# Optimization experiments

Measured on AMD Instinct MI355X. Metric: run time of the kernel, lower is better.

The kernel has to match this reference:

```python
import jax, jax.numpy as jnp
import numpy as np

NEG_INF = -1e30


def setup_inputs() -> dict:
    key = jax.random.key(0)
    ks = jax.random.split(key, 5)
    B, S, D, H = 2, 2048, 1024, 16
    sc = 0.02  # weight init scale
    return {
        "x": jax.random.normal(ks[0], (B, S, D), dtype=jnp.float32),
        "Wq": jax.random.normal(ks[1], (D, D), dtype=jnp.float32) * sc,
        "bq": jnp.zeros((D,), dtype=jnp.float32),
        "Wk": jax.random.normal(ks[2], (D, D), dtype=jnp.float32) * sc,
        "bk": jnp.zeros((D,), dtype=jnp.float32),
        "Wv": jax.random.normal(ks[3], (D, D), dtype=jnp.float32) * sc,
        "bv": jnp.zeros((D,), dtype=jnp.float32),
        "Wo": jax.random.normal(ks[4], (D, D), dtype=jnp.float32) * sc,
        "bo": jnp.zeros((D,), dtype=jnp.float32),
        "temperature": jnp.ones((H,), dtype=jnp.float32),
    }


def reference(x, Wq, bq, Wk, bk, Wv, bv, Wo, bo, temperature):
    B, S, D = x.shape
    H = temperature.shape[0]
    hd = D // H
    sparsity = 0.8
    k = max(1, int(S * (1.0 - sparsity)))
    scale = hd ** (-0.5)

    # torch Linear: y = x @ W^T + b ; reshape to [B, S, H, hd] -> [B, H, S, hd]
    def proj(W, b):
        return (x @ W.T + b).reshape(B, S, H, hd).transpose(0, 2, 1, 3)

    q, kk, v = proj(Wq, bq), proj(Wk, bk), proj(Wv, bv)

    temp = jnp.clip(temperature, 0.1, None)[None, :, None, None]  # [1,H,1,1]
    scores = jnp.einsum("bhqd,bhkd->bhqk", q, kk) * scale / temp  # [B,H,S,S]

    # top-k sparsity: keep the k largest scores per row, -inf elsewhere.
    # Equivalent to torch's topk+scatter for distinct values: threshold at
    # the k-th largest value per row.
    topk_vals = jax.lax.top_k(scores, k)[0]           # [B,H,S,k]
    kth = topk_vals[..., -1:]                          # [B,H,S,1]
    sparse_scores = jnp.where(scores >= kth, scores, NEG_INF)

    attn = jax.nn.softmax(sparse_scores, axis=-1)      # [B,H,S,S]
    head_out = jnp.einsum("bhqk,bhkd->bhqd", attn, v)  # [B,H,S,hd]

    # stack heads back: [B,S,H,hd] -> [B,S,D], then out projection
    out = head_out.transpose(0, 2, 1, 3).reshape(B, S, D)
    out = out @ Wo.T + bo

    avg_attention = attn.mean(axis=1)                  # [B,S,S]
    return out, avg_attention
```

## Files before the change

kernel.cpp:

```cpp
#include <hip/hip_runtime.h>
#include <stdint.h>

#define S_LEN 2048
#define D_DIM 1024
#define NHEAD 16
#define HD    64
#define TOPK  409

typedef unsigned short u16;
typedef __attribute__((ext_vector_type(8))) short bf16x8;
typedef __attribute__((ext_vector_type(4))) float f32x4;
#define MFMA __builtin_amdgcn_mfma_f32_16x16x32_bf16

__device__ __forceinline__ u16 f2b(float f) {
    unsigned u = __float_as_uint(f);
    return (u16)((u + 0x7fffu + ((u >> 16) & 1u)) >> 16);
}
__device__ __forceinline__ float b2f(u16 h) {
    return __uint_as_float(((unsigned)h) << 16);
}

__global__ __launch_bounds__(256, 4)
void split_f32(const float* __restrict__ src, u16* __restrict__ hi,
               u16* __restrict__ lo, int n4)
{
    const int i = blockIdx.x * 256 + threadIdx.x;
    if (i >= n4) return;
    const float4 v = ((const float4*)src)[i];
    const float vv[4] = {v.x, v.y, v.z, v.w};
    u16 h4[4], l4[4];
#pragma unroll
    for (int c = 0; c < 4; ++c) {
        h4[c] = f2b(vv[c]);
        l4[c] = f2b(vv[c] - b2f(h4[c]));
    }
    ((ushort4*)hi)[i] = make_ushort4(h4[0], h4[1], h4[2], h4[3]);
    ((ushort4*)lo)[i] = make_ushort4(l4[0], l4[1], l4[2], l4[3]);
}

__global__ __launch_bounds__(256, 4)
void split4_f32(const float* __restrict__ s0, const float* __restrict__ s1,
                const float* __restrict__ s2, const float* __restrict__ s3,
                u16* __restrict__ h0, u16* __restrict__ l0,
                u16* __restrict__ h1, u16* __restrict__ l1,
                u16* __restrict__ h2, u16* __restrict__ l2,
                u16* __restrict__ h3, u16* __restrict__ l3, int n4)
{
    const int i = blockIdx.x * 256 + threadIdx.x;
    if (i >= n4) return;
    const int y = blockIdx.y;
    const float* src = (y == 0) ? s0 : (y == 1) ? s1 : (y == 2) ? s2 : s3;
    u16* hi = (y == 0) ? h0 : (y == 1) ? h1 : (y == 2) ? h2 : h3;
    u16* lo = (y == 0) ? l0 : (y == 1) ? l1 : (y == 2) ? l2 : l3;
    const float4 v = ((const float4*)src)[i];
    const float vv[4] = {v.x, v.y, v.z, v.w};
    u16 h4[4], l4[4];
#pragma unroll
    for (int c = 0; c < 4; ++c) {
        h4[c] = f2b(vv[c]);
        l4[c] = f2b(vv[c] - b2f(h4[c]));
    }
    ((ushort4*)hi)[i] = make_ushort4(h4[0], h4[1], h4[2], h4[3]);
    ((ushort4*)lo)[i] = make_ushort4(l4[0], l4[1], l4[2], l4[3]);
}

template<int MODE>
__global__ __launch_bounds__(512, 2)
void proj_mfma(const u16* __restrict__ Ahi, const u16* __restrict__ Alo,
               const u16* __restrict__ Whi, const u16* __restrict__ Wlo,
               const float* __restrict__ bias, float* __restrict__ outf,
               u16* __restrict__ o1, u16* __restrict__ o2)
{
    const int t = threadIdx.x, w = t >> 6, l = t & 63;
    const int lq = l & 15, quad = l >> 4;
    const int m0 = blockIdx.y * 128 + (w >> 2) * 64;
    const int n0 = blockIdx.x * 128 + (w & 3) * 32;

    f32x4 acc[4][2];
#pragma unroll
    for (int i = 0; i < 4; ++i)
#pragma unroll
        for (int j = 0; j < 2; ++j) acc[i][j] = (f32x4){0.f, 0.f, 0.f, 0.f};

    const size_t abase = (size_t)(m0 + lq) * D_DIM + quad * 8;
    const size_t bbase = (size_t)(n0 + lq) * D_DIM + quad * 8;

#pragma unroll 2
    for (int k0 = 0; k0 < D_DIM; k0 += 32) {
        bf16x8 ah[4], al[4], bh[2], bl[2];
#pragma unroll
        for (int i = 0; i < 4; ++i) {
            ah[i] = *(const bf16x8*)(Ahi + abase + (size_t)i * 16 * D_DIM + k0);
            al[i] = *(const bf16x8*)(Alo + abase + (size_t)i * 16 * D_DIM + k0);
        }
#pragma unroll
        for (int j = 0; j < 2; ++j) {
            bh[j] = *(const bf16x8*)(Whi + bbase + (size_t)j * 16 * D_DIM + k0);
            bl[j] = *(const bf16x8*)(Wlo + bbase + (size_t)j * 16 * D_DIM + k0);
        }
#pragma unroll
        for (int i = 0; i < 4; ++i)
#pragma unroll
            for (int j = 0; j < 2; ++j) {
                acc[i][j] = MFMA(ah[i], bh[j], acc[i][j], 0, 0, 0);
                acc[i][j] = MFMA(ah[i], bl[j], acc[i][j], 0, 0, 0);
                acc[i][j] = MFMA(al[i], bh[j], acc[i][j], 0, 0, 0);
            }
    }

#pragma unroll
    for (int j = 0; j < 2; ++j) {
        const int n = n0 + j * 16 + lq;
        const float bb = bias[n];
        const int hh = n >> 6, ee = n & 63;
#pragma unroll
        for (int i = 0; i < 4; ++i) {
            const int mb = m0 + i * 16 + quad * 4;
            const int bbm = mb >> 11, ss = mb & 2047;
            if (MODE == 2) {
#pragma unroll
                for (int r = 0; r < 4; ++r)
                    outf[(size_t)(mb + r) * D_DIM + n] = acc[i][j][r] + bb;
            } else if (MODE == 1) {
                ushort4 pk;
                pk.x = f2b(acc[i][j][0] + bb);
                pk.y = f2b(acc[i][j][1] + bb);
                pk.z = f2b(acc[i][j][2] + bb);
                pk.w = f2b(acc[i][j][3] + bb);
                *(ushort4*)(o1 + ((size_t)((bbm * NHEAD + hh) * HD + ee)) * S_LEN + ss) = pk;
            } else {
#pragma unroll
                for (int r = 0; r < 4; ++r) {
                    const float v = acc[i][j][r] + bb;
                    const size_t idx = ((size_t)(bbm * NHEAD + hh) * S_LEN + ss + r) * HD + ee;
                    const u16 h = f2b(v);
                    o1[idx] = h;
                    o2[idx] = f2b(v - b2f(h));
                }
            }
        }
    }
}

__global__ __launch_bounds__(512, 4)
void attn_mfma(const u16* __restrict__ Qhi, const u16* __restrict__ Qlo,
               const u16* __restrict__ Khi, const u16* __restrict__ Klo,
               const u16* __restrict__ Vt,  const float* __restrict__ temp,
               u16* __restrict__ HOhi, u16* __restrict__ HOlo,
               float* __restrict__ avg)
{
    __shared__ __align__(16) float sLds[8 * 2060];
    __shared__ float pvpart[4 * 16 * 16];

    const int t = threadIdx.x, w = t >> 6, l = t & 63;
    const int lq = l & 15, quad = l >> 4;
    const int b  = blockIdx.x >> 8;
    const int q0 = (blockIdx.x & 255) << 3;

    float avgreg[32];
#pragma unroll
    for (int i = 0; i < 32; ++i) avgreg[i] = 0.f;

#pragma unroll 1
    for (int h = 0; h < NHEAD; ++h) {
        const size_t bh = (size_t)(b * NHEAD + h) * S_LEN;
        const float tscale = 0.125f / fmaxf(temp[h], 0.1f);

        const u16* qph = Qhi + (bh + q0 + (lq & 7)) * HD + quad * 8;
        const u16* qpl = Qlo + (bh + q0 + (lq & 7)) * HD + quad * 8;
        const bf16x8 qh0 = *(const bf16x8*)qph;
        const bf16x8 qh1 = *(const bf16x8*)(qph + 32);
        const bf16x8 ql0 = *(const bf16x8*)qpl;
        const bf16x8 ql1 = *(const bf16x8*)(qpl + 32);

#pragma unroll 1
        for (int p = 0; p < 2; ++p) {
            f32x4 acc[8];
            const u16* kph = Khi + (bh + p * 1024 + w * 128 + lq) * HD + quad * 8;
            const u16* kpl = Klo + (bh + p * 1024 + w * 128 + lq) * HD + quad * 8;
#pragma unroll
            for (int tt = 0; tt < 8; ++tt) {
                const bf16x8 k0 = *(const bf16x8*)(kph + tt * 16 * HD);
                const bf16x8 k1 = *(const bf16x8*)(kph + tt * 16 * HD + 32);
                const bf16x8 m0 = *(const bf16x8*)(kpl + tt * 16 * HD);
                const bf16x8 m1 = *(const bf16x8*)(kpl + tt * 16 * HD + 32);
                f32x4 a = {0.f, 0.f, 0.f, 0.f};
                a = MFMA(qh0, k0, a, 0, 0, 0);
                a = MFMA(qh1, k1, a, 0, 0, 0);
                a = MFMA(qh0, m0, a, 0, 0, 0);
                a = MFMA(qh1, m1, a, 0, 0, 0);
                a = MFMA(ql0, k0, a, 0, 0, 0);
                a = MFMA(ql1, k1, a, 0, 0, 0);
                acc[tt] = a * tscale;
            }
            if (quad < 2) {
#pragma unroll
                for (int tt = 0; tt < 8; ++tt)
#pragma unroll
                    for (int r = 0; r < 4; ++r)
                        sLds[(quad * 4 + r) * 2060 + p * 1024 + w * 128 + tt * 16 + lq]
                            = acc[tt][r];
            }
        }
        __syncthreads();

        float s[32];
        {
            const float* srow = sLds + (size_t)w * 2060 + 2 * l;
#pragma unroll
            for (int j = 0; j < 16; ++j) {
                const float2 p = *(const float2*)(srow + 128 * j);
                s[2 * j]     = p.x;
                s[2 * j + 1] = p.y;
            }
        }

        float s1 = 0.f, s2 = 0.f;
#pragma unroll
        for (int j = 0; j < 32; ++j) { s1 += s[j]; s2 = __fmaf_rn(s[j], s[j], s2); }
#pragma unroll
        for (int off = 1; off < 64; off <<= 1) {
            s1 += __shfl_xor(s1, off, 64);
            s2 += __shfl_xor(s2, off, 64);
        }
        const float mu = s1 * (1.f / 2048.f);
        const float va = s2 * (1.f / 2048.f) - mu * mu;
        const float sg = sqrtf(fmaxf(va, 0.f));

        float lo, hi;
        {
            float th[5];
            int c[5];
#pragma unroll
            for (int i = 0; i < 5; ++i) {
                th[i] = __fmaf_rn(sg, 0.55f + 0.15f * (float)i, mu);
                c[i] = 0;
            }
#pragma unroll
            for (int j = 0; j < 32; ++j) {
                const float v = s[j];
#pragma unroll
                for (int i = 0; i < 5; ++i) c[i] += (v >= th[i]) ? 1 : 0;
            }
#pragma unroll
            for (int off = 1; off < 64; off <<= 1)
#pragma unroll
                for (int i = 0; i < 5; ++i) c[i] += __shfl_xor(c[i], off, 64);
            if (c[0] < TOPK) {
                lo = __fmaf_rn(sg, -6.f, mu);
                hi = th[0];
            } else if (c[4] >= TOPK) {
                lo = th[4];
                hi = __fmaf_rn(sg, 6.f, mu);
            } else {
                int bi = 0;
#pragma unroll
                for (int j = 1; j < 4; ++j) if (c[j] >= TOPK) bi = j;
                lo = th[bi];
                hi = th[bi + 1];
            }
        }

#pragma unroll 1
        for (int rd = 0; rd < 5; ++rd) {
            const float w4 = __fmul_rn(__fsub_rn(hi, lo), 0.25f);
            const float t1 = __fmaf_rn(w4, 1.f, lo);
            const float t2 = __fmaf_rn(w4, 2.f, lo);
            const float t3 = __fmaf_rn(w4, 3.f, lo);
            int d0 = 0, d1 = 0, d2 = 0;
#pragma unroll
            for (int j = 0; j < 32; ++j) {
                const float v = s[j];
                d0 += (v >= t1) ? 1 : 0;
                d1 += (v >= t2) ? 1 : 0;
                d2 += (v >= t3) ? 1 : 0;
            }
#pragma unroll
            for (int off = 1; off < 64; off <<= 1) {
                d0 += __shfl_xor(d0, off, 64);
                d1 += __shfl_xor(d1, off, 64);
                d2 += __shfl_xor(d2, off, 64);
            }
            if (d2 >= TOPK)      { lo = t3; }
            else if (d1 >= TOPK) { lo = t2; hi = t3; }
            else if (d0 >= TOPK) { lo = t1; hi = t2; }
            else                 { hi = t1; }
        }

        const float kth = lo;
        float zp = 0.f;
#pragma unroll
        for (int j = 0; j < 32; ++j) {
            const float e = (s[j] >= kth) ? __expf(s[j]) : 0.f;
            s[j] = e;
            zp += e;
        }
#pragma unroll
        for (int off = 1; off < 64; off <<= 1) zp += __shfl_xor(zp, off, 64);
        const float zi = 1.f / zp;

        {
            u16* arow = (u16*)(sLds + (size_t)w * 2060);
#pragma unroll
            for (int j = 0; j < 16; ++j) {
                const float a0 = s[2 * j] * zi;
                const float a1 = s[2 * j + 1] * zi;
                avgreg[2 * j]     += a0;
                avgreg[2 * j + 1] += a1;
                const unsigned pk = (unsigned)f2b(a0) | ((unsigned)f2b(a1) << 16);
                *(unsigned*)(arow + 2 * l + 128 * j) = pk;
            }
        }
        __syncthreads();

        const int et = w & 3, jh = w >> 2;
        const u16* vb = Vt + ((size_t)(b * NHEAD + h) * HD + et * 16 + lq) * S_LEN
                        + jh * 1024 + quad * 8;
        const u16* ab = (const u16*)sLds + (size_t)(lq & 7) * 4120 + jh * 1024 + quad * 8;
        f32x4 pv = {0.f, 0.f, 0.f, 0.f};
#pragma unroll 8
        for (int st = 0; st < 32; ++st) {
            const bf16x8 af = *(const bf16x8*)(ab + st * 32);
            const bf16x8 vf = *(const bf16x8*)(vb + st * 32);
            pv = MFMA(af, vf, pv, 0, 0, 0);
        }
        if (w >= 4) {
#pragma unroll
            for (int r = 0; r < 4; ++r)
                pvpart[(et * 16 + quad * 4 + r) * 16 + lq] = pv[r];
        }
        __syncthreads();
        if (w < 4 && quad < 2) {
#pragma unroll
            for (int r = 0; r < 4; ++r) {
                const float v = pv[r] + pvpart[(et * 16 + quad * 4 + r) * 16 + lq];
                const size_t idx =
                    ((size_t)(b * S_LEN + q0 + quad * 4 + r)) * D_DIM + h * HD + et * 16 + lq;
                const u16 hv = f2b(v);
                HOhi[idx] = hv;
                HOlo[idx] = f2b(v - b2f(hv));
            }
        }
    }

    float* avrow = avg + ((size_t)(b * S_LEN + q0 + w)) * S_LEN + 2 * l;
#pragma unroll
    for (int j = 0; j < 16; ++j) {
        float2 o;
        o.x = avgreg[2 * j]     * (1.f / NHEAD);
        o.y = avgreg[2 * j + 1] * (1.f / NHEAD);
        *(float2*)(avrow + 128 * j) = o;
    }
}

extern "C" void kernel_launch(void* const* d_in, const int* in_sizes, int n_in,
                              void* d_out, int out_size, void* d_ws, size_t ws_size,
                              hipStream_t stream)
{
    const float* x    = (const float*)d_in[0];
    const float* Wq   = (const float*)d_in[1];
    const float* bq   = (const float*)d_in[2];
    const float* Wk   = (const float*)d_in[3];
    const float* bk   = (const float*)d_in[4];
    const float* Wv   = (const float*)d_in[5];
    const float* bv   = (const float*)d_in[6];
    const float* Wo   = (const float*)d_in[7];
    const float* bo   = (const float*)d_in[8];
    const float* temp = (const float*)d_in[9];
    float* out = (float*)d_out;

    const int B = in_sizes[0] / (S_LEN * D_DIM);
    const int M = B * S_LEN;
    const size_t NQ = (size_t)M * D_DIM;
    const size_t NW = (size_t)D_DIM * D_DIM;

    u16* Qhi = (u16*)d_ws;
    u16* Qlo = Qhi + NQ;
    u16* Khi = Qlo + NQ;
    u16* Klo = Khi + NQ;
    u16* Vt  = Klo + NQ;
    u16* Xhi = Vt  + NQ;
    u16* Xlo = Xhi + NQ;
    u16* Wqh = Xlo + NQ;
    u16* Wql = Wqh + NW;
    u16* Wkh = Wql + NW;
    u16* Wkl = Wkh + NW;
    u16* Wvh = Wkl + NW;
    u16* Wvl = Wvh + NW;
    u16* Woh = Wvl + NW;
    u16* Wol = Woh + NW;
    float* avg = out + NQ;

    const int n4x = (int)(NQ / 4), n4w = (int)(NW / 4);
    split_f32<<<(n4x + 255) / 256, 256, 0, stream>>>(x, Xhi, Xlo, n4x);
    split4_f32<<<dim3((n4w + 255) / 256, 4), 256, 0, stream>>>(
        Wq, Wk, Wv, Wo, Wqh, Wql, Wkh, Wkl, Wvh, Wvl, Woh, Wol, n4w);

    dim3 gg(D_DIM / 128, M / 128, 1);
    proj_mfma<0><<<gg, 512, 0, stream>>>(Xhi, Xlo, Wqh, Wql, bq, nullptr, Qhi, Qlo);
    proj_mfma<0><<<gg, 512, 0, stream>>>(Xhi, Xlo, Wkh, Wkl, bk, nullptr, Khi, Klo);
    proj_mfma<1><<<gg, 512, 0, stream>>>(Xhi, Xlo, Wvh, Wvl, bv, nullptr, Vt, nullptr);

    attn_mfma<<<dim3(M / 8), 512, 0, stream>>>(Qhi, Qlo, Khi, Klo, Vt, temp,
                                               Xhi, Xlo, avg);

    proj_mfma<2><<<gg, 512, 0, stream>>>(Xhi, Xlo, Woh, Wol, bo, out, nullptr, nullptr);
}
```

Baseline: 1.235 ms.

## Process 16 query rows per attention block with 1024 threads

The attention kernel now covers 16 queries per block instead of 8, using 16 waves. Each wave computes a 128-key slice of QK^T, which fills all 16 MFMA rows where half were previously wasted. PV is split four ways over keys and reduced through a padded LDS buffer. This doubles the LDS footprint per block and the block size, which may reduce how many blocks fit per CU, and adds a larger cross-wave reduction.

```diff
diff --git a/kernel.cpp b/kernel.cpp
--- a/kernel.cpp
+++ b/kernel.cpp
@@ -142,20 +142,20 @@
     }
 }
 
-__global__ __launch_bounds__(512, 4)
+__global__ __launch_bounds__(1024, 4)
 void attn_mfma(const u16* __restrict__ Qhi, const u16* __restrict__ Qlo,
                const u16* __restrict__ Khi, const u16* __restrict__ Klo,
                const u16* __restrict__ Vt,  const float* __restrict__ temp,
                u16* __restrict__ HOhi, u16* __restrict__ HOlo,
                float* __restrict__ avg)
 {
-    __shared__ __align__(16) float sLds[8 * 2060];
-    __shared__ float pvpart[4 * 16 * 16];
+    __shared__ __align__(16) float sLds[16 * 2060];
+    __shared__ float pvpart[3][64][17];
 
     const int t = threadIdx.x, w = t >> 6, l = t & 63;
     const int lq = l & 15, quad = l >> 4;
-    const int b  = blockIdx.x >> 8;
-    const int q0 = (blockIdx.x & 255) << 3;
+    const int b  = blockIdx.x >> 7;
+    const int q0 = (blockIdx.x & 127) << 4;
 
     float avgreg[32];
 #pragma unroll
@@ -166,42 +166,37 @@
         const size_t bh = (size_t)(b * NHEAD + h) * S_LEN;
         const float tscale = 0.125f / fmaxf(temp[h], 0.1f);
 
-        const u16* qph = Qhi + (bh + q0 + (lq & 7)) * HD + quad * 8;
-        const u16* qpl = Qlo + (bh + q0 + (lq & 7)) * HD + quad * 8;
+        const u16* qph = Qhi + (bh + q0 + lq) * HD + quad * 8;
+        const u16* qpl = Qlo + (bh + q0 + lq) * HD + quad * 8;
         const bf16x8 qh0 = *(const bf16x8*)qph;
         const bf16x8 qh1 = *(const bf16x8*)(qph + 32);
         const bf16x8 ql0 = *(const bf16x8*)qpl;
         const bf16x8 ql1 = *(const bf16x8*)(qpl + 32);
 
-#pragma unroll 1
-        for (int p = 0; p < 2; ++p) {
-            f32x4 acc[8];
-            const u16* kph = Khi + (bh + p * 1024 + w * 128 + lq) * HD + quad * 8;
-            const u16* kpl = Klo + (bh + p * 1024 + w * 128 + lq) * HD + quad * 8;
-#pragma unroll
-            for (int tt = 0; tt < 8; ++tt) {
-                const bf16x8 k0 = *(const bf16x8*)(kph + tt * 16 * HD);
-                const bf16x8 k1 = *(const bf16x8*)(kph + tt * 16 * HD + 32);
-                const bf16x8 m0 = *(const bf16x8*)(kpl + tt * 16 * HD);
-                const bf16x8 m1 = *(const bf16x8*)(kpl + tt * 16 * HD + 32);
-                f32x4 a = {0.f, 0.f, 0.f, 0.f};
-                a = MFMA(qh0, k0, a, 0, 0, 0);
-                a = MFMA(qh1, k1, a, 0, 0, 0);
-                a = MFMA(qh0, m0, a, 0, 0, 0);
-                a = MFMA(qh1, m1, a, 0, 0, 0);
-                a = MFMA(ql0, k0, a, 0, 0, 0);
-                a = MFMA(ql1, k1, a, 0, 0, 0);
-                acc[tt] = a * tscale;
-            }
-            if (quad < 2) {
-#pragma unroll
-                for (int tt = 0; tt < 8; ++tt)
-#pragma unroll
-                    for (int r = 0; r < 4; ++r)
-                        sLds[(quad * 4 + r) * 2060 + p * 1024 + w * 128 + tt * 16 + lq]
-                            = acc[tt][r];
-            }
-        }
+        f32x4 acc[8];
+        const u16* kph = Khi + (bh + w * 128 + lq) * HD + quad * 8;
+        const u16* kpl = Klo + (bh + w * 128 + lq) * HD + quad * 8;
+#pragma unroll
+        for (int tt = 0; tt < 8; ++tt) {
+            const bf16x8 k0 = *(const bf16x8*)(kph + tt * 16 * HD);
+            const bf16x8 k1 = *(const bf16x8*)(kph + tt * 16 * HD + 32);
+            const bf16x8 m0 = *(const bf16x8*)(kpl + tt * 16 * HD);
+            const bf16x8 m1 = *(const bf16x8*)(kpl + tt * 16 * HD + 32);
+            f32x4 a = {0.f, 0.f, 0.f, 0.f};
+            a = MFMA(qh0, k0, a, 0, 0, 0);
+            a = MFMA(qh1, k1, a, 0, 0, 0);
+            a = MFMA(qh0, m0, a, 0, 0, 0);
+            a = MFMA(qh1, m1, a, 0, 0, 0);
+            a = MFMA(ql0, k0, a, 0, 0, 0);
+            a = MFMA(ql1, k1, a, 0, 0, 0);
+            acc[tt] = a * tscale;
+        }
+
+#pragma unroll
+        for (int tt = 0; tt < 8; ++tt)
+#pragma unroll
+            for (int r = 0; r < 4; ++r)
+                sLds[(quad * 4 + r) * 2060 + w * 128 + tt * 16 + lq] = acc[tt][r];
         __syncthreads();
 
         float s[32];
@@ -313,27 +308,29 @@
         }
         __syncthreads();
 
-        const int et = w & 3, jh = w >> 2;
+        const int et = w & 3, jq = w >> 2;
         const u16* vb = Vt + ((size_t)(b * NHEAD + h) * HD + et * 16 + lq) * S_LEN
-                        + jh * 1024 + quad * 8;
-        const u16* ab = (const u16*)sLds + (size_t)(lq & 7) * 4120 + jh * 1024 + quad * 8;
+                        + jq * 512 + quad * 8;
+        const u16* ab = (const u16*)sLds + (size_t)lq * 4120 + jq * 512 + quad * 8;
         f32x4 pv = {0.f, 0.f, 0.f, 0.f};
 #pragma unroll 8
-        for (int st = 0; st < 32; ++st) {
+        for (int st = 0; st < 16; ++st) {
             const bf16x8 af = *(const bf16x8*)(ab + st * 32);
             const bf16x8 vf = *(const bf16x8*)(vb + st * 32);
             pv = MFMA(af, vf, pv, 0, 0, 0);
         }
-        if (w >= 4) {
+        if (jq > 0) {
 #pragma unroll
             for (int r = 0; r < 4; ++r)
-                pvpart[(et * 16 + quad * 4 + r) * 16 + lq] = pv[r];
+                pvpart[jq - 1][et * 16 + quad * 4 + r][lq] = pv[r];
         }
         __syncthreads();
-        if (w < 4 && quad < 2) {
+        if (jq == 0) {
 #pragma unroll
             for (int r = 0; r < 4; ++r) {
-                const float v = pv[r] + pvpart[(et * 16 + quad * 4 + r) * 16 + lq];
+                const int row = et * 16 + quad * 4 + r;
+                const float v = pv[r] + pvpart[0][row][lq] + pvpart[1][row][lq]
+                              + pvpart[2][row][lq];
                 const size_t idx =
                     ((size_t)(b * S_LEN + q0 + quad * 4 + r)) * D_DIM + h * HD + et * 16 + lq;
                 const u16 hv = f2b(v);
@@ -401,8 +398,8 @@
     proj_mfma<0><<<gg, 512, 0, stream>>>(Xhi, Xlo, Wkh, Wkl, bk, nullptr, Khi, Klo);
     proj_mfma<1><<<gg, 512, 0, stream>>>(Xhi, Xlo, Wvh, Wvl, bv, nullptr, Vt, nullptr);
 
-    attn_mfma<<<dim3(M / 8), 512, 0, stream>>>(Qhi, Qlo, Khi, Klo, Vt, temp,
-                                               Xhi, Xlo, avg);
+    attn_mfma<<<dim3(M / 16), 1024, 0, stream>>>(Qhi, Qlo, Khi, Klo, Vt, temp,
+                                                 Xhi, Xlo, avg);
 
     proj_mfma<2><<<gg, 512, 0, stream>>>(Xhi, Xlo, Woh, Wol, bo, out, nullptr, nullptr);
 }
```

New measurement: 1.085 ms. 12.1% less time.
